# Performance work log

Hardware: AMD Instinct MI355X
Metric: run time of the kernel (lower is better)

## Reference

```python
import jax, jax.numpy as jnp
import numpy as np

EPS = 1e-5

def layer_norm(x, g, b):
    m = jnp.mean(x, axis=-1, keepdims=True)
    v = jnp.var(x, axis=-1, keepdims=True)
    return (x - m) * jax.lax.rsqrt(v + EPS) * g + b

def setup_inputs() -> dict:
    key = jax.random.key(0)
    ks = jax.random.split(key, 16)
    B, N, C_Z, C_H = 1, 512, 128, 128
    s_z = 1.0 / np.sqrt(C_Z)
    s_h = 1.0 / np.sqrt(C_H)
    inp = {
        "z": jax.random.normal(ks[0], (B, N, N, C_Z), jnp.float32),
        "mask": jnp.ones((B, N, N), jnp.float32),
        # linear weights stored as [in, out] so forward is x @ W + b
        "w_ag": jax.random.uniform(ks[1], (C_Z, C_H), jnp.float32, -s_z, s_z),
        "b_ag": jnp.zeros((C_H,), jnp.float32),
        "w_ap": jax.random.uniform(ks[2], (C_Z, C_H), jnp.float32, -s_z, s_z),
        "b_ap": jnp.zeros((C_H,), jnp.float32),
        "w_bg": jax.random.uniform(ks[3], (C_Z, C_H), jnp.float32, -s_z, s_z),
        "b_bg": jnp.zeros((C_H,), jnp.float32),
        "w_bp": jax.random.uniform(ks[4], (C_Z, C_H), jnp.float32, -s_z, s_z),
        "b_bp": jnp.zeros((C_H,), jnp.float32),
        "w_g": jax.random.uniform(ks[5], (C_Z, C_Z), jnp.float32, -s_z, s_z),
        "b_g": jnp.zeros((C_Z,), jnp.float32),
        "w_z": jax.random.uniform(ks[6], (C_H, C_Z), jnp.float32, -s_h, s_h),
        "b_z": jnp.zeros((C_Z,), jnp.float32),
        "ln_in_g": jnp.ones((C_Z,), jnp.float32),
        "ln_in_b": jnp.zeros((C_Z,), jnp.float32),
        "ln_out_g": jnp.ones((C_H,), jnp.float32),
        "ln_out_b": jnp.zeros((C_H,), jnp.float32),
    }
    return inp

def reference(z, mask, w_ag, b_ag, w_ap, b_ap, w_bg, b_bg, w_bp, b_bp,
              w_g, b_g, w_z, b_z, ln_in_g, ln_in_b, ln_out_g, ln_out_b):
    m = mask[..., None]                      # [B,N,N,1]
    zn = layer_norm(z, ln_in_g, ln_in_b)     # [B,N,N,Cz]
    a = m * jax.nn.sigmoid(zn @ w_ag + b_ag) * (zn @ w_ap + b_ap)  # [B,N,N,Ch]
    b = m * jax.nn.sigmoid(zn @ w_bg + b_bg) * (zn @ w_bp + b_bp)  # [B,N,N,Ch]
    # outgoing: p[i,j,c] = sum_k a[i,k,c] * b[j,k,c]
    x = jnp.einsum('bikc,bjkc->bijc', a, b)
    x = layer_norm(x, ln_out_g, ln_out_b)
    x = x @ w_z + b_z
    g = jax.nn.sigmoid(zn @ w_g + b_g)
    return x * g
```

## Files before the change

kernel.cpp:

```cpp
#include <hip/hip_runtime.h>
#include <hip/hip_bf16.h>
#include <math.h>


#define N 512
#define C 128
#define NN (N*N)
#define PK 136
#define PX 137
#define ST 72

typedef __attribute__((ext_vector_type(8))) short bf16x8;
typedef __attribute__((ext_vector_type(4))) float f32x4;
typedef unsigned short u16;
typedef unsigned int u32;

__device__ __forceinline__ u16 f2bf(float f) {
    u32 u = __builtin_bit_cast(u32, f);
    u = (u + 0x7fffu + ((u >> 16) & 1u)) >> 16;
    return (u16)u;
}
__device__ __forceinline__ float bf2f(u16 h) {
    return __builtin_bit_cast(float, ((u32)h) << 16);
}
__device__ __forceinline__ float sigmoidf(float x) {
    return 1.f / (1.f + __expf(-x));
}
__device__ __forceinline__ void gload16(const u16* g, u16* lds) {
    __builtin_amdgcn_global_load_lds(
        (const __attribute__((address_space(1))) unsigned int*)g,
        (__attribute__((address_space(3))) unsigned int*)lds, 16, 0, 0);
}

__global__ __launch_bounds__(256) void k_wt_all(
    const float* __restrict__ w0, const float* __restrict__ w1,
    const float* __restrict__ w2, const float* __restrict__ w3,
    const float* __restrict__ w4, const float* __restrict__ w5,
    const float* __restrict__ gin, const float* __restrict__ gout,
    u16* __restrict__ o0, u16* __restrict__ o1, u16* __restrict__ o2,
    u16* __restrict__ o3, u16* __restrict__ o4, u16* __restrict__ o5) {
    int sel = blockIdx.x >> 6;
    int idx = (blockIdx.x & 63) * 256 + threadIdx.x;
    const float* w = sel == 0 ? w0 : sel == 1 ? w1 : sel == 2 ? w2
                   : sel == 3 ? w3 : sel == 4 ? w4 : w5;
    u16* o = sel == 0 ? o0 : sel == 1 ? o1 : sel == 2 ? o2
           : sel == 3 ? o3 : sel == 4 ? o4 : o5;
    const float* g = (sel == 5) ? gout : gin;
    int co = idx >> 7, k = idx & 127;
    o[idx] = f2bf(g[k] * w[k * C + co]);
}

__global__ __launch_bounds__(256) void k_bias(
    const float* __restrict__ w0, const float* __restrict__ w1,
    const float* __restrict__ w2, const float* __restrict__ w3,
    const float* __restrict__ w4, const float* __restrict__ w5,
    const float* __restrict__ b0, const float* __restrict__ b1,
    const float* __restrict__ b2, const float* __restrict__ b3,
    const float* __restrict__ b4, const float* __restrict__ b5,
    const float* __restrict__ vin, const float* __restrict__ vout,
    float* __restrict__ obias) {
    int id = blockIdx.x * 256 + threadIdx.x;
    int m = id >> 7, cc = id & 127;
    const float* w = m == 0 ? w0 : m == 1 ? w1 : m == 2 ? w2
                   : m == 3 ? w3 : m == 4 ? w4 : w5;
    const float* b = m == 0 ? b0 : m == 1 ? b1 : m == 2 ? b2
                   : m == 3 ? b3 : m == 4 ? b4 : b5;
    const float* v = (m == 5) ? vout : vin;
    float acc = 0.f;
#pragma unroll 4
    for (int k = 0; k < 128; ++k) acc += v[k] * w[k * C + cc];
    obias[id] = b[cc] + acc;
}

__global__ __launch_bounds__(256, 2) void k_proj_fused(
    const float* __restrict__ z, const float* __restrict__ mask,
    const u16* __restrict__ wag, const u16* __restrict__ wap,
    const u16* __restrict__ wbg, const u16* __restrict__ wbp,
    const u16* __restrict__ wgg, const float* __restrict__ biasAll,
    u16* __restrict__ aT, u16* __restrict__ bT, u16* __restrict__ gate) {
    __shared__ u16 sA[64 * PK];
    __shared__ u16 sT[4][2][16 * ST];
    long r0 = (long)blockIdx.x * 64;
    int tid = threadIdx.x, wave = tid >> 6, lane = tid & 63;
    int lo = lane & 15, quad = lane >> 4;

    {
        int rl = lane >> 2, cb = lane & 3;
        int row = wave * 16 + rl;
        const float* zr = z + (r0 + row) * C + cb * 32;
        float4 v[8];
        float s = 0.f, s2 = 0.f;
#pragma unroll
        for (int i = 0; i < 8; ++i) {
            v[i] = *(const float4*)(zr + i * 4);
            s  += v[i].x + v[i].y + v[i].z + v[i].w;
            s2 += v[i].x * v[i].x + v[i].y * v[i].y + v[i].z * v[i].z + v[i].w * v[i].w;
        }
        s += __shfl_xor(s, 1); s2 += __shfl_xor(s2, 1);
        s += __shfl_xor(s, 2); s2 += __shfl_xor(s2, 2);
        float mean = s * (1.f / 128.f);
        float rs = rsqrtf(s2 * (1.f / 128.f) - mean * mean + 1e-5f);
        u16* dst = &sA[row * PK + cb * 32];
#pragma unroll
        for (int j = 0; j < 4; ++j) {
            uint4 pk;
            pk.x = (u32)f2bf((v[2*j].x   - mean) * rs) | ((u32)f2bf((v[2*j].y   - mean) * rs) << 16);
            pk.y = (u32)f2bf((v[2*j].z   - mean) * rs) | ((u32)f2bf((v[2*j].w   - mean) * rs) << 16);
            pk.z = (u32)f2bf((v[2*j+1].x - mean) * rs) | ((u32)f2bf((v[2*j+1].y - mean) * rs) << 16);
            pk.w = (u32)f2bf((v[2*j+1].z - mean) * rs) | ((u32)f2bf((v[2*j+1].w - mean) * rs) << 16);
            *(uint4*)(dst + 8 * j) = pk;
        }
    }
    __syncthreads();

    int c0 = wave * 32;
    float msk[4][4];
#pragma unroll
    for (int mi = 0; mi < 4; ++mi)
#pragma unroll
        for (int r = 0; r < 4; ++r)
            msk[mi][r] = mask[r0 + mi * 16 + quad * 4 + r];

    auto epi = [&](const f32x4* G, const f32x4* P, float bGv, float bPv,
                   u16* sTh, u16* __restrict__ outT, int cch) {
#pragma unroll
        for (int mi = 0; mi < 4; ++mi) {
            float v0 = msk[mi][0] * sigmoidf(G[mi][0] + bGv) * (P[mi][0] + bPv);
            float v1 = msk[mi][1] * sigmoidf(G[mi][1] + bGv) * (P[mi][1] + bPv);
            float v2 = msk[mi][2] * sigmoidf(G[mi][2] + bGv) * (P[mi][2] + bPv);
            float v3 = msk[mi][3] * sigmoidf(G[mi][3] + bGv) * (P[mi][3] + bPv);
            uint2 pk;
            pk.x = (u32)f2bf(v0) | ((u32)f2bf(v1) << 16);
            pk.y = (u32)f2bf(v2) | ((u32)f2bf(v3) << 16);
            *(uint2*)(&sTh[lo * ST + mi * 16 + quad * 4]) = pk;
        }
        int cl = lane >> 2, pr = lane & 3;
        uint4 x0 = *(const uint4*)(&sTh[cl * ST + pr * 16]);
        uint4 x1 = *(const uint4*)(&sTh[cl * ST + pr * 16 + 8]);
        u16* g = outT + (long)(cch + cl) * NN + r0 + pr * 16;
        *(uint4*)(g) = x0;
        *(uint4*)(g + 8) = x1;
    };

    f32x4 gG[2][4];
#pragma unroll
    for (int nt = 0; nt < 2; ++nt)
#pragma unroll
        for (int mi = 0; mi < 4; ++mi) gG[nt][mi] = (f32x4)(0.f);

#pragma unroll
    for (int nt = 0; nt < 2; ++nt) {
        int c = c0 + nt * 16 + lo;
        bf16x8 fAG[4], fAP[4], fBG[4], fBP[4], fGG[4];
#pragma unroll
        for (int ki = 0; ki < 4; ++ki) {
            fAG[ki] = *(const bf16x8*)(wag + c * C + ki * 32 + quad * 8);
            fAP[ki] = *(const bf16x8*)(wap + c * C + ki * 32 + quad * 8);
            fBG[ki] = *(const bf16x8*)(wbg + c * C + ki * 32 + quad * 8);
            fBP[ki] = *(const bf16x8*)(wbp + c * C + ki * 32 + quad * 8);
            fGG[ki] = *(const bf16x8*)(wgg + c * C + ki * 32 + quad * 8);
        }
        f32x4 aG[4], aP[4], bG[4], bP[4];
#pragma unroll
        for (int mi = 0; mi < 4; ++mi) {
            aG[mi] = (f32x4)(0.f); aP[mi] = (f32x4)(0.f);
            bG[mi] = (f32x4)(0.f); bP[mi] = (f32x4)(0.f);
        }
#pragma unroll
        for (int mi = 0; mi < 4; ++mi)
#pragma unroll
            for (int ki = 0; ki < 4; ++ki) {
                bf16x8 av = *(const bf16x8*)(&sA[(mi * 16 + lo) * PK + ki * 32 + quad * 8]);
                aG[mi]     = __builtin_amdgcn_mfma_f32_16x16x32_bf16(av, fAG[ki], aG[mi], 0, 0, 0);
                aP[mi]     = __builtin_amdgcn_mfma_f32_16x16x32_bf16(av, fAP[ki], aP[mi], 0, 0, 0);
                bG[mi]     = __builtin_amdgcn_mfma_f32_16x16x32_bf16(av, fBG[ki], bG[mi], 0, 0, 0);
                bP[mi]     = __builtin_amdgcn_mfma_f32_16x16x32_bf16(av, fBP[ki], bP[mi], 0, 0, 0);
                gG[nt][mi] = __builtin_amdgcn_mfma_f32_16x16x32_bf16(av, fGG[ki], gG[nt][mi], 0, 0, 0);
            }
        epi(aG, aP, biasAll[c],       biasAll[128 + c], &sT[wave][0][0], aT, c0 + nt * 16);
        epi(bG, bP, biasAll[256 + c], biasAll[384 + c], &sT[wave][1][0], bT, c0 + nt * 16);
    }

    __syncthreads();
    const float* bg5 = biasAll + 512;
#pragma unroll
    for (int nt = 0; nt < 2; ++nt) {
        int c = c0 + nt * 16 + lo;
        float bv = bg5[c];
#pragma unroll
        for (int mi = 0; mi < 4; ++mi)
#pragma unroll
            for (int r = 0; r < 4; ++r)
                sA[(mi * 16 + quad * 4 + r) * PK + c] = f2bf(sigmoidf(gG[nt][mi][r] + bv));
    }
    __syncthreads();
#pragma unroll
    for (int p = 0; p < 4; ++p) {
        int linear = p * 2048 + tid * 8;
        int row = linear >> 7, k = linear & 127;
        *(uint4*)(gate + (r0 + row) * C + k) = *(const uint4*)(&sA[row * PK + k]);
    }
}

__global__ __launch_bounds__(256) void k_tri(const u16* __restrict__ aT,
                                             const u16* __restrict__ bT,
                                             u16* __restrict__ xT) {
    __shared__ u16 sA[128 * 32];
    __shared__ u16 sB[128 * 32];
    int c = blockIdx.y;
    int i0 = (blockIdx.x >> 2) * 128, j0 = (blockIdx.x & 3) * 128;
    const u16* aBase = aT + (long)c * NN + (long)i0 * N;
    const u16* bBase = bT + (long)c * NN + (long)j0 * N;
    int tid = threadIdx.x;
    int wave = tid >> 6, lane = tid & 63, lo = lane & 15, quad = lane >> 4;
    int mq = (wave >> 1) * 64, nq = (wave & 1) * 64;
    int ld_row = lane >> 2;
    int ld_col = (lane & 3) * 8;
    f32x4 acc[4][4];
#pragma unroll
    for (int mi = 0; mi < 4; ++mi)
#pragma unroll
        for (int ni = 0; ni < 4; ++ni) acc[mi][ni] = (f32x4)(0.f);
    for (int kk = 0; kk < N; kk += 32) {
        __syncthreads();
#pragma unroll
        for (int h = 0; h < 2; ++h) {
            int ch = wave + h * 4;
            int r = ch * 16 + ld_row;
            gload16(aBase + (long)r * N + kk + ld_col, &sA[ch * 512]);
            gload16(bBase + (long)r * N + kk + ld_col, &sB[ch * 512]);
        }
        __syncthreads();
        bf16x8 af[4], bfr[4];
#pragma unroll
        for (int mi = 0; mi < 4; ++mi)
            af[mi] = *(const bf16x8*)(&sA[(mq + mi * 16 + lo) * 32 + quad * 8]);
#pragma unroll
        for (int ni = 0; ni < 4; ++ni)
            bfr[ni] = *(const bf16x8*)(&sB[(nq + ni * 16 + lo) * 32 + quad * 8]);
#pragma unroll
        for (int mi = 0; mi < 4; ++mi)
#pragma unroll
            for (int ni = 0; ni < 4; ++ni)
                acc[mi][ni] = __builtin_amdgcn_mfma_f32_16x16x32_bf16(af[mi], bfr[ni], acc[mi][ni], 0, 0, 0);
    }
    u16* outBase = xT + (long)c * NN;
#pragma unroll
    for (int mi = 0; mi < 4; ++mi)
#pragma unroll
        for (int ni = 0; ni < 4; ++ni)
#pragma unroll
            for (int r = 0; r < 4; ++r) {
                int gi = i0 + mq + mi * 16 + quad * 4 + r;
                int gj = j0 + nq + ni * 16 + lo;
                outBase[(long)gi * N + gj] = f2bf(acc[mi][ni][r]);
            }
}

__global__ __launch_bounds__(256) void k_out(
    const u16* __restrict__ xT, const u16* __restrict__ gate,
    const u16* __restrict__ wzT, const float* __restrict__ bz,
    float* __restrict__ out) {
    __shared__ float sX[64 * PX];
    __shared__ u16 sA[64 * PK];
    __shared__ float sRed[2][4][64];
    __shared__ float2 sMV[64];
    long r0 = (long)blockIdx.x * 64;
    int tid = threadIdx.x;
#pragma unroll
    for (int p = 0; p < 4; ++p) {
        int linear = p * 2048 + tid * 8;
        int cc = linear >> 6, jr = linear & 63;
        uint4 v = *(const uint4*)(xT + (long)cc * NN + r0 + jr);
        u16* u = (u16*)&v;
#pragma unroll
        for (int e = 0; e < 8; ++e) sX[(jr + e) * PX + cc] = bf2f(u[e]);
    }
    __syncthreads();
    {
        int jr = tid & 63, part = tid >> 6;
        float s = 0, s2 = 0;
#pragma unroll
        for (int c = part * 32; c < part * 32 + 32; ++c) {
            float v = sX[jr * PX + c];
            s += v; s2 += v * v;
        }
        sRed[0][part][jr] = s; sRed[1][part][jr] = s2;
    }
    __syncthreads();
    if (tid < 64) {
        float S = 0, S2 = 0;
#pragma unroll
        for (int p = 0; p < 4; ++p) { S += sRed[0][p][tid]; S2 += sRed[1][p][tid]; }
        float mean = S * (1.f / 128.f);
        float var = S2 * (1.f / 128.f) - mean * mean;
        sMV[tid] = make_float2(mean, rsqrtf(var + 1e-5f));
    }
    __syncthreads();
    {
        int row = tid & 63, c0 = (tid >> 6) * 32;
        float2 mv = sMV[row];
#pragma unroll
        for (int c = c0; c < c0 + 32; ++c)
            sA[row * PK + c] = f2bf((sX[row * PX + c] - mv.x) * mv.y);
    }
    __syncthreads();
    int wave = tid >> 6, lane = tid & 63, lo = lane & 15, quad = lane >> 4;
    int msub = wave * 16;
    bf16x8 av[4];
#pragma unroll
    for (int ki = 0; ki < 4; ++ki)
        av[ki] = *(const bf16x8*)(&sA[(msub + lo) * PK + ki * 32 + quad * 8]);
    f32x4 acc[8];
#pragma unroll
    for (int nt = 0; nt < 8; ++nt) acc[nt] = (f32x4)(0.f);
#pragma unroll
    for (int nt = 0; nt < 8; ++nt)
#pragma unroll
        for (int ki = 0; ki < 4; ++ki) {
            bf16x8 b8 = *(const bf16x8*)(wzT + (nt * 16 + lo) * C + ki * 32 + quad * 8);
            acc[nt] = __builtin_amdgcn_mfma_f32_16x16x32_bf16(av[ki], b8, acc[nt], 0, 0, 0);
        }
#pragma unroll
    for (int nt = 0; nt < 8; ++nt) {
        int c = nt * 16 + lo;
        float bzv = bz[c];
#pragma unroll
        for (int r = 0; r < 4; ++r) {
            int row = msub + quad * 4 + r;
            long rr = r0 + row;
            float g = bf2f(gate[rr * C + c]);
            out[rr * C + c] = (acc[nt][r] + bzv) * g;
        }
    }
}

extern "C" void kernel_launch(void* const* d_in, const int* in_sizes, int n_in,
                              void* d_out, int out_size, void* d_ws, size_t ws_size,
                              hipStream_t stream) {
    const float* z       = (const float*)d_in[0];
    const float* mask    = (const float*)d_in[1];
    const float* w_ag    = (const float*)d_in[2];
    const float* b_ag    = (const float*)d_in[3];
    const float* w_ap    = (const float*)d_in[4];
    const float* b_ap    = (const float*)d_in[5];
    const float* w_bg    = (const float*)d_in[6];
    const float* b_bg    = (const float*)d_in[7];
    const float* w_bp    = (const float*)d_in[8];
    const float* b_bp    = (const float*)d_in[9];
    const float* w_g     = (const float*)d_in[10];
    const float* b_g     = (const float*)d_in[11];
    const float* w_z     = (const float*)d_in[12];
    const float* b_z     = (const float*)d_in[13];
    const float* ln_in_g = (const float*)d_in[14];
    const float* ln_in_b = (const float*)d_in[15];
    const float* ln_out_g= (const float*)d_in[16];
    const float* ln_out_b= (const float*)d_in[17];
    float* out = (float*)d_out;

    char* ws = (char*)d_ws;
    u16* a_t  = (u16*)(ws);
    u16* b_t  = (u16*)(ws + 67108864L);
    u16* gate = (u16*)(ws + 134217728L);
    u16* x_t  = (u16*)(ws + 201326592L);
    u16* wag_t = (u16*)(ws + 268435456L);
    u16* wap_t = wag_t + 16384;
    u16* wbg_t = wag_t + 32768;
    u16* wbp_t = wag_t + 49152;
    u16* wg_t  = wag_t + 65536;
    u16* wz_t  = wag_t + 81920;
    float* biasAdj = (float*)(ws + 268435456L + 196608L);

    k_wt_all<<<384, 256, 0, stream>>>(w_ag, w_ap, w_bg, w_bp, w_g, w_z,
                                      ln_in_g, ln_out_g,
                                      wag_t, wap_t, wbg_t, wbp_t, wg_t, wz_t);

    k_bias<<<3, 256, 0, stream>>>(w_ag, w_ap, w_bg, w_bp, w_g, w_z,
                                  b_ag, b_ap, b_bg, b_bp, b_g, b_z,
                                  ln_in_b, ln_out_b, biasAdj);

    k_proj_fused<<<NN / 64, 256, 0, stream>>>(
        z, mask, wag_t, wap_t, wbg_t, wbp_t, wg_t, biasAdj,
        a_t, b_t, gate);

    k_tri<<<dim3(16, 128), 256, 0, stream>>>(a_t, b_t, x_t);

    k_out<<<NN / 64, 256, 0, stream>>>(x_t, gate, wz_t, biasAdj + 640, out);
}
```

Baseline: 558.4 us.

## Double-buffer triangle GEMM tiles and fold output layernorm into GEMM epilogue

The triangle-multiply kernel now uses two shared-memory buffers, so the next k-tile is loaded while the current one feeds the MFMAs, and one barrier per iteration is dropped. The output kernel stores raw bf16 x directly and skips the normalized copy pass. The mean and rstd of the output layernorm are applied after the projection GEMM, using a precomputed column sum of the gamma-scaled Wz weights, which k_bias now also produces. This cuts LDS traffic and a barrier in k_out. The risk is different rounding, since un-normalized x enters the bf16 MFMA and the mean subtraction happens after accumulation.

```diff
diff --git a/kernel.cpp b/kernel.cpp
--- a/kernel.cpp
+++ b/kernel.cpp
@@ -7,7 +7,6 @@
 #define C 128
 #define NN (N*N)
 #define PK 136
-#define PX 137
 #define ST 72
 
 typedef __attribute__((ext_vector_type(8))) short bf16x8;
@@ -58,9 +57,19 @@
     const float* __restrict__ b2, const float* __restrict__ b3,
     const float* __restrict__ b4, const float* __restrict__ b5,
     const float* __restrict__ vin, const float* __restrict__ vout,
+    const float* __restrict__ gout,
     float* __restrict__ obias) {
     int id = blockIdx.x * 256 + threadIdx.x;
     int m = id >> 7, cc = id & 127;
+    if (m >= 7) return;
+    if (m == 6) {
+        float acc = 0.f;
+#pragma unroll 4
+        for (int k = 0; k < 128; ++k)
+            acc += bf2f(f2bf(gout[k] * w5[k * C + cc]));
+        obias[id] = acc;
+        return;
+    }
     const float* w = m == 0 ? w0 : m == 1 ? w1 : m == 2 ? w2
                    : m == 3 ? w3 : m == 4 ? w4 : w5;
     const float* b = m == 0 ? b0 : m == 1 ? b1 : m == 2 ? b2
@@ -205,8 +214,8 @@
 __global__ __launch_bounds__(256) void k_tri(const u16* __restrict__ aT,
                                              const u16* __restrict__ bT,
                                              u16* __restrict__ xT) {
-    __shared__ u16 sA[128 * 32];
-    __shared__ u16 sB[128 * 32];
+    __shared__ u16 sA[2][128 * 32];
+    __shared__ u16 sB[2][128 * 32];
     int c = blockIdx.y;
     int i0 = (blockIdx.x >> 2) * 128, j0 = (blockIdx.x & 3) * 128;
     const u16* aBase = aT + (long)c * NN + (long)i0 * N;
@@ -216,33 +225,44 @@
     int mq = (wave >> 1) * 64, nq = (wave & 1) * 64;
     int ld_row = lane >> 2;
     int ld_col = (lane & 3) * 8;
-    f32x4 acc[4][4];
-#pragma unroll
-    for (int mi = 0; mi < 4; ++mi)
-#pragma unroll
-        for (int ni = 0; ni < 4; ++ni) acc[mi][ni] = (f32x4)(0.f);
-    for (int kk = 0; kk < N; kk += 32) {
-        __syncthreads();
+
+    auto stage = [&](int t, int buf) {
 #pragma unroll
         for (int h = 0; h < 2; ++h) {
             int ch = wave + h * 4;
             int r = ch * 16 + ld_row;
-            gload16(aBase + (long)r * N + kk + ld_col, &sA[ch * 512]);
-            gload16(bBase + (long)r * N + kk + ld_col, &sB[ch * 512]);
-        }
-        __syncthreads();
+            gload16(aBase + (long)r * N + t * 32 + ld_col, &sA[buf][ch * 512]);
+            gload16(bBase + (long)r * N + t * 32 + ld_col, &sB[buf][ch * 512]);
+        }
+    };
+
+    f32x4 acc[4][4];
+#pragma unroll
+    for (int mi = 0; mi < 4; ++mi)
+#pragma unroll
+        for (int ni = 0; ni < 4; ++ni) acc[mi][ni] = (f32x4)(0.f);
+
+    stage(0, 0);
+    __syncthreads();
+    int cur = 0;
+    for (int t = 0; t < 16; ++t) {
+        if (t + 1 < 16) stage(t + 1, cur ^ 1);
         bf16x8 af[4], bfr[4];
 #pragma unroll
         for (int mi = 0; mi < 4; ++mi)
-            af[mi] = *(const bf16x8*)(&sA[(mq + mi * 16 + lo) * 32 + quad * 8]);
+            af[mi] = *(const bf16x8*)(&sA[cur][(mq + mi * 16 + lo) * 32 + quad * 8]);
 #pragma unroll
         for (int ni = 0; ni < 4; ++ni)
-            bfr[ni] = *(const bf16x8*)(&sB[(nq + ni * 16 + lo) * 32 + quad * 8]);
+            bfr[ni] = *(const bf16x8*)(&sB[cur][(nq + ni * 16 + lo) * 32 + quad * 8]);
 #pragma unroll
         for (int mi = 0; mi < 4; ++mi)
 #pragma unroll
             for (int ni = 0; ni < 4; ++ni)
                 acc[mi][ni] = __builtin_amdgcn_mfma_f32_16x16x32_bf16(af[mi], bfr[ni], acc[mi][ni], 0, 0, 0);
+        if (t + 1 < 16) {
+            __syncthreads();
+            cur ^= 1;
+        }
     }
     u16* outBase = xT + (long)c * NN;
 #pragma unroll
@@ -260,8 +280,8 @@
 __global__ __launch_bounds__(256) void k_out(
     const u16* __restrict__ xT, const u16* __restrict__ gate,
     const u16* __restrict__ wzT, const float* __restrict__ bz,
+    const float* __restrict__ colsum,
     float* __restrict__ out) {
-    __shared__ float sX[64 * PX];
     __shared__ u16 sA[64 * PK];
     __shared__ float sRed[2][4][64];
     __shared__ float2 sMV[64];
@@ -274,22 +294,24 @@
         uint4 v = *(const uint4*)(xT + (long)cc * NN + r0 + jr);
         u16* u = (u16*)&v;
 #pragma unroll
-        for (int e = 0; e < 8; ++e) sX[(jr + e) * PX + cc] = bf2f(u[e]);
+        for (int e = 0; e < 8; ++e) sA[(jr + e) * PK + cc] = u[e];
     }
     __syncthreads();
     {
         int jr = tid & 63, part = tid >> 6;
-        float s = 0, s2 = 0;
-#pragma unroll
-        for (int c = part * 32; c < part * 32 + 32; ++c) {
-            float v = sX[jr * PX + c];
-            s += v; s2 += v * v;
+        float s = 0.f, s2 = 0.f;
+#pragma unroll
+        for (int q = 0; q < 4; ++q) {
+            uint4 w = *(const uint4*)(&sA[jr * PK + part * 32 + q * 8]);
+            const u16* uu = (const u16*)&w;
+#pragma unroll
+            for (int e = 0; e < 8; ++e) { float v = bf2f(uu[e]); s += v; s2 += v * v; }
         }
         sRed[0][part][jr] = s; sRed[1][part][jr] = s2;
     }
     __syncthreads();
     if (tid < 64) {
-        float S = 0, S2 = 0;
+        float S = 0.f, S2 = 0.f;
 #pragma unroll
         for (int p = 0; p < 4; ++p) { S += sRed[0][p][tid]; S2 += sRed[1][p][tid]; }
         float mean = S * (1.f / 128.f);
@@ -297,14 +319,6 @@
         sMV[tid] = make_float2(mean, rsqrtf(var + 1e-5f));
     }
     __syncthreads();
-    {
-        int row = tid & 63, c0 = (tid >> 6) * 32;
-        float2 mv = sMV[row];
-#pragma unroll
-        for (int c = c0; c < c0 + 32; ++c)
-            sA[row * PK + c] = f2bf((sX[row * PX + c] - mv.x) * mv.y);
-    }
-    __syncthreads();
     int wave = tid >> 6, lane = tid & 63, lo = lane & 15, quad = lane >> 4;
     int msub = wave * 16;
     bf16x8 av[4];
@@ -321,16 +335,19 @@
             bf16x8 b8 = *(const bf16x8*)(wzT + (nt * 16 + lo) * C + ki * 32 + quad * 8);
             acc[nt] = __builtin_amdgcn_mfma_f32_16x16x32_bf16(av[ki], b8, acc[nt], 0, 0, 0);
         }
+    float2 mvr[4];
+#pragma unroll
+    for (int r = 0; r < 4; ++r) mvr[r] = sMV[msub + quad * 4 + r];
 #pragma unroll
     for (int nt = 0; nt < 8; ++nt) {
-        int c = nt * 16 + lo;
-        float bzv = bz[c];
+        int cch = nt * 16 + lo;
+        float bzv = bz[cch], csv = colsum[cch];
 #pragma unroll
         for (int r = 0; r < 4; ++r) {
             int row = msub + quad * 4 + r;
             long rr = r0 + row;
-            float g = bf2f(gate[rr * C + c]);
-            out[rr * C + c] = (acc[nt][r] + bzv) * g;
+            float g = bf2f(gate[rr * C + cch]);
+            out[rr * C + cch] = (mvr[r].y * (acc[nt][r] - mvr[r].x * csv) + bzv) * g;
         }
     }
 }
@@ -375,9 +392,9 @@
                                       ln_in_g, ln_out_g,
                                       wag_t, wap_t, wbg_t, wbp_t, wg_t, wz_t);
 
-    k_bias<<<3, 256, 0, stream>>>(w_ag, w_ap, w_bg, w_bp, w_g, w_z,
+    k_bias<<<4, 256, 0, stream>>>(w_ag, w_ap, w_bg, w_bp, w_g, w_z,
                                   b_ag, b_ap, b_bg, b_bp, b_g, b_z,
-                                  ln_in_b, ln_out_b, biasAdj);
+                                  ln_in_b, ln_out_b, ln_out_g, biasAdj);
 
     k_proj_fused<<<NN / 64, 256, 0, stream>>>(
         z, mask, wag_t, wap_t, wbg_t, wbp_t, wg_t, biasAdj,
@@ -385,5 +402,6 @@
 
     k_tri<<<dim3(16, 128), 256, 0, stream>>>(a_t, b_t, x_t);
 
-    k_out<<<NN / 64, 256, 0, stream>>>(x_t, gate, wz_t, biasAdj + 640, out);
-}
+    k_out<<<NN / 64, 256, 0, stream>>>(x_t, gate, wz_t, biasAdj + 640,
+                                       biasAdj + 768, out);
+}
```

After: 558.0 us. No clear change (-0.1%).
